# Kernel tuning notes

Hardware: AMD Instinct MI355X
Metric: run time of the kernel (lower is better)

## Reference

```python
import jax, jax.numpy as jnp
import numpy as np

B, H, S, D = 2, 16, 2048, 64

def setup_inputs() -> dict:
    key = jax.random.key(0)
    kq, kk, kv = jax.random.split(key, 3)
    q = jax.random.normal(kq, (B, H, S, D), dtype=jnp.float32)
    k = jax.random.normal(kk, (B, H, S, D), dtype=jnp.float32)
    v = jax.random.normal(kv, (B, H, S, D), dtype=jnp.float32)
    mask = jnp.tril(jnp.ones((S, S), dtype=bool))  # causal, broadcast over B,H
    return {"q": q, "k": k, "v": v, "mask": mask}

def reference(q, k, v, mask):
    d_k = q.shape[-1]
    # [..., num_q, num_kv]
    qk = jnp.einsum('bhqd,bhkd->bhqk', q, k) / jnp.sqrt(jnp.asarray(d_k, q.dtype))
    qk = jnp.where(mask, qk, -jnp.inf)
    attn = jax.nn.softmax(qk, axis=-1)
    return jnp.einsum('bhqk,bhkd->bhqd', attn, v)
```

## Files before the change

kernel.cpp:

```cpp
#include <hip/hip_runtime.h>

#define SS 2048
#define DD 64
#define BH 32
#define QSCALE 0.1803368801f
#define BUFS 8448

typedef __attribute__((ext_vector_type(8))) short short8;
typedef __attribute__((ext_vector_type(4))) float floatx4;

__device__ __forceinline__ short f2bf(float x) {
  union { float f; unsigned u; } un; un.f = x;
  unsigned r = (un.u + 0x7FFFu + ((un.u >> 16) & 1u)) >> 16;
  return (short)r;
}
__device__ __forceinline__ float fexp2(float x) {
  return __builtin_amdgcn_exp2f(x);
}
__device__ __forceinline__ void gload16(const short* g, short* l) {
  __builtin_amdgcn_global_load_lds(
      (const __attribute__((address_space(1))) void*)g,
      (__attribute__((address_space(3))) void*)l, 16, 0, 0);
}
#define MFMA __builtin_amdgcn_mfma_f32_16x16x32_bf16

__device__ __forceinline__ int kperm(int c) {
  return (((c >> 2) & 1) << 4) + ((c >> 3) << 2) + (c & 3);
}

__global__ __launch_bounds__(256) void prep_kv(const float* __restrict__ K,
                                               const float* __restrict__ V,
                                               short* __restrict__ Kbf,
                                               short* __restrict__ Vtp) {
  __shared__ short Ts[64][72];
  const int bh = blockIdx.x;
  const int r0 = blockIdx.y * 64;
  const int t  = threadIdx.x;
  {
    const int r = t >> 2, c = (t & 3) * 16;
    const float* g = V + ((size_t)bh * SS + r0 + r) * DD + c;
    floatx4 a = *(const floatx4*)g;
    floatx4 b = *(const floatx4*)(g + 4);
    floatx4 cc = *(const floatx4*)(g + 8);
    floatx4 dd = *(const floatx4*)(g + 12);
    short8 x0, x1;
    x0[0]=f2bf(a[0]); x0[1]=f2bf(a[1]); x0[2]=f2bf(a[2]); x0[3]=f2bf(a[3]);
    x0[4]=f2bf(b[0]); x0[5]=f2bf(b[1]); x0[6]=f2bf(b[2]); x0[7]=f2bf(b[3]);
    x1[0]=f2bf(cc[0]);x1[1]=f2bf(cc[1]);x1[2]=f2bf(cc[2]);x1[3]=f2bf(cc[3]);
    x1[4]=f2bf(dd[0]);x1[5]=f2bf(dd[1]);x1[6]=f2bf(dd[2]);x1[7]=f2bf(dd[3]);
    *(short8*)&Ts[r][c] = x0;
    *(short8*)&Ts[r][c + 8] = x1;
  }
  {
    const size_t i = ((size_t)bh * SS + r0) * DD + (size_t)t * 16;
    floatx4 a = *(const floatx4*)(K + i);
    floatx4 b = *(const floatx4*)(K + i + 4);
    floatx4 cc = *(const floatx4*)(K + i + 8);
    floatx4 dd = *(const floatx4*)(K + i + 12);
    short8 x0, x1;
    x0[0]=f2bf(a[0]); x0[1]=f2bf(a[1]); x0[2]=f2bf(a[2]); x0[3]=f2bf(a[3]);
    x0[4]=f2bf(b[0]); x0[5]=f2bf(b[1]); x0[6]=f2bf(b[2]); x0[7]=f2bf(b[3]);
    x1[0]=f2bf(cc[0]);x1[1]=f2bf(cc[1]);x1[2]=f2bf(cc[2]);x1[3]=f2bf(cc[3]);
    x1[4]=f2bf(dd[0]);x1[5]=f2bf(dd[1]);x1[6]=f2bf(dd[2]);x1[7]=f2bf(dd[3]);
    *(short8*)(Kbf + i) = x0;
    *(short8*)(Kbf + i + 8) = x1;
  }
  __syncthreads();
  {
    const int d = t >> 2, cblk = (t & 3) * 16;
    short8 y0, y1;
    #pragma unroll
    for (int jj = 0; jj < 8; ++jj) {
      const int c0 = cblk + jj, c1 = cblk + 8 + jj;
      y0[jj] = Ts[(c0 & 32) + kperm(c0 & 31)][d];
      y1[jj] = Ts[(c1 & 32) + kperm(c1 & 31)][d];
    }
    const int kt  = (r0 + cblk) >> 5;
    const int kin = cblk & 31;
    short* o = Vtp + (((size_t)bh * 64 + kt) * 64 + d) * 32 + kin;
    *(short8*)o = y0;
    *(short8*)(o + 8) = y1;
  }
}

#define CVTPK(DST_, A_, B_) \
  __asm__("v_cvt_pk_bf16_f32 %0, %1, %2" : "=v"(DST_) : "v"(A_), "v"(B_))

#define TILE32(JJ, DIAG_)                                                    \
  {                                                                          \
    const short* lb = bufp + (JJ) * 2176;                                    \
    const short* vb = bufp + 4352 + (JJ) * 2048;                             \
    short8 kb00 = *(const short8*)(lb + kroA);                               \
    short8 kb01 = *(const short8*)(lb + kroB);                               \
    short8 kb10 = *(const short8*)(lb + kroA + 1088);                        \
    short8 kb11 = *(const short8*)(lb + kroB + 1088);                        \
    short8 vt0 = *(const short8*)(vb + vro);                                 \
    short8 vt1 = *(const short8*)(vb + vro + 512);                           \
    short8 vt2 = *(const short8*)(vb + vro + 1024);                          \
    short8 vt3 = *(const short8*)(vb + vro + 1536);                          \
    __builtin_amdgcn_s_setprio(1);                                           \
    floatx4 tA0 = z, tA1 = z, tB0 = z, tB1 = z;                              \
    tA0 = MFMA(kb00, qaA0, tA0, 0, 0, 0); tA0 = MFMA(kb01, qaA1, tA0, 0, 0, 0);\
    tA1 = MFMA(kb10, qaA0, tA1, 0, 0, 0); tA1 = MFMA(kb11, qaA1, tA1, 0, 0, 0);\
    tB0 = MFMA(kb00, qaB0, tB0, 0, 0, 0); tB0 = MFMA(kb01, qaB1, tB0, 0, 0, 0);\
    tB1 = MFMA(kb10, qaB0, tB1, 0, 0, 0); tB1 = MFMA(kb11, qaB1, tB1, 0, 0, 0);\
    if (DIAG_) {                                                             \
      _Pragma("unroll")                                                      \
      for (int r = 0; r < 4; ++r) {                                          \
        tA0[r] = (quad * 4 + r      <= l16) ? tA0[r] : -1e30f;               \
        tA1[r] = (quad * 4 + r + 16 <= l16) ? tA1[r] : -1e30f;               \
        tB1[r] = (quad * 4 + r      <= l16) ? tB1[r] : -1e30f;               \
      }                                                                      \
    }                                                                        \
    _Pragma("unroll")                                                        \
    for (int r = 0; r < 4; ++r) {                                            \
      tA0[r] = fexp2(tA0[r]); tA1[r] = fexp2(tA1[r]);                        \
      tB0[r] = fexp2(tB0[r]); tB1[r] = fexp2(tB1[r]);                        \
    }                                                                        \
    union { unsigned u[4]; short8 s; } upA, upB;                             \
    CVTPK(upA.u[0], tA0[0], tA0[1]); CVTPK(upA.u[1], tA0[2], tA0[3]);        \
    CVTPK(upA.u[2], tA1[0], tA1[1]); CVTPK(upA.u[3], tA1[2], tA1[3]);        \
    CVTPK(upB.u[0], tB0[0], tB0[1]); CVTPK(upB.u[1], tB0[2], tB0[3]);        \
    CVTPK(upB.u[2], tB1[0], tB1[1]); CVTPK(upB.u[3], tB1[2], tB1[3]);        \
    short8 paA = upA.s, paB = upB.s;                                         \
    sA = MFMA(ones, paA, sA, 0, 0, 0);                                       \
    sB = MFMA(ones, paB, sB, 0, 0, 0);                                       \
    oA0 = MFMA(vt0, paA, oA0, 0, 0, 0); oA1 = MFMA(vt1, paA, oA1, 0, 0, 0);  \
    oA2 = MFMA(vt2, paA, oA2, 0, 0, 0); oA3 = MFMA(vt3, paA, oA3, 0, 0, 0);  \
    oB0 = MFMA(vt0, paB, oB0, 0, 0, 0); oB1 = MFMA(vt1, paB, oB1, 0, 0, 0);  \
    oB2 = MFMA(vt2, paB, oB2, 0, 0, 0); oB3 = MFMA(vt3, paB, oB3, 0, 0, 0);  \
    __builtin_amdgcn_s_setprio(0);                                           \
  }

__global__ __launch_bounds__(256, 4) void sdpa_fused(
    const float* __restrict__ Q, const short* __restrict__ Kbf,
    const short* __restrict__ Vtp, float* __restrict__ Og) {
  __shared__ __align__(16) short Sh[2][BUFS];

  const int tid  = threadIdx.x;
  const int w    = tid >> 6;
  const int lane = tid & 63;
  const int quad = lane >> 4;
  const int l16  = lane & 15;
  const int qp   = w >> 1;
  const int kp   = w & 1;

  const int bh = blockIdx.x;
  const int y  = blockIdx.y;
  const int qt = (y < 16) ? (31 - y) : (y - 16);

  const size_t base = (size_t)bh * SS * DD;
  const short* kbase = Kbf + base;
  const short* vtb   = Vtp + base;

  const int kso = (lane >> 3) * 64 + (((lane & 7) ^ (lane >> 3)) * 8);
  const int vso = (lane >> 2) * 32 + (((lane & 3) ^ ((lane >> 3) & 3)) * 8);
  const int kroA = (l16 >> 3) * 544 + (l16 & 7) * 64 + ((quad ^ (l16 & 7)) * 8);
  const int kroB = (l16 >> 3) * 544 + (l16 & 7) * 64 + (((quad + 4) ^ (l16 & 7)) * 8);
  const int vro  = l16 * 32 + ((quad ^ ((l16 >> 1) & 3)) * 8);

  short8 ones;
  #pragma unroll
  for (int r = 0; r < 8; ++r) ones[r] = (short)0x3F80;
  const floatx4 z = {0.f, 0.f, 0.f, 0.f};

  const int np = qt + 1;
  const int qA = qt * 64 + qp * 32;
  const int qB = qA + 16;

  {
    const short* gk = kbase + w * 512 + kso;
    gload16(gk,        &Sh[0][w * 544]);
    gload16(gk + 2048, &Sh[0][2176 + w * 544]);
    const short* gv = vtb + w * 512 + vso;
    gload16(gv,        &Sh[0][4352 + w * 512]);
    gload16(gv + 2048, &Sh[0][6400 + w * 512]);
  }

  short8 qaA0, qaA1, qaB0, qaB1;
  {
    const float* ga = Q + base + (size_t)(qA + l16) * DD + quad * 8;
    const float* gb = Q + base + (size_t)(qB + l16) * DD + quad * 8;
    floatx4 a0 = *(const floatx4*)ga,        a1 = *(const floatx4*)(ga + 4);
    floatx4 a2 = *(const floatx4*)(ga + 32), a3 = *(const floatx4*)(ga + 36);
    floatx4 b0 = *(const floatx4*)gb,        b1 = *(const floatx4*)(gb + 4);
    floatx4 b2 = *(const floatx4*)(gb + 32), b3 = *(const floatx4*)(gb + 36);
    #pragma unroll
    for (int r = 0; r < 4; ++r) {
      qaA0[r] = f2bf(a0[r] * QSCALE); qaA0[4 + r] = f2bf(a1[r] * QSCALE);
      qaA1[r] = f2bf(a2[r] * QSCALE); qaA1[4 + r] = f2bf(a3[r] * QSCALE);
      qaB0[r] = f2bf(b0[r] * QSCALE); qaB0[4 + r] = f2bf(b1[r] * QSCALE);
      qaB1[r] = f2bf(b2[r] * QSCALE); qaB1[4 + r] = f2bf(b3[r] * QSCALE);
    }
  }

  floatx4 oA0 = z, oA1 = z, oA2 = z, oA3 = z;
  floatx4 oB0 = z, oB1 = z, oB2 = z, oB3 = z;
  floatx4 sA = z, sB = z;

  int nb = 0;
  for (int p = 0; p < np; ++p) {
    __asm__ volatile("s_waitcnt vmcnt(0)" ::: "memory");
    __syncthreads();
    const short* bufp = Sh[nb];

    if (p + 1 < np) {
      {
        const size_t go = (size_t)(p + 1) * 4096;
        const short* gk = kbase + go + w * 512 + kso;
        gload16(gk,        &Sh[nb ^ 1][w * 544]);
        gload16(gk + 2048, &Sh[nb ^ 1][2176 + w * 544]);
        const short* gv = vtb + go + w * 512 + vso;
        gload16(gv,        &Sh[nb ^ 1][4352 + w * 512]);
        gload16(gv + 2048, &Sh[nb ^ 1][6400 + w * 512]);
      }
      TILE32(kp, 0)
    } else {
      if (kp == qp) { TILE32(kp, 1) }
      else if (kp < qp) { TILE32(kp, 0) }
    }
    nb ^= 1;
  }

  __syncthreads();
  float* lf = (float*)&Sh[0][0];
  if (kp) {
    floatx4* dst = (floatx4*)&lf[qp * 2048];
    dst[0 * 64 + lane] = oA0; dst[1 * 64 + lane] = oA1;
    dst[2 * 64 + lane] = oA2; dst[3 * 64 + lane] = oA3;
    dst[4 * 64 + lane] = oB0; dst[5 * 64 + lane] = oB1;
    dst[6 * 64 + lane] = oB2; dst[7 * 64 + lane] = oB3;
    lf[4096 + qp * 128 + lane]      = sA[0];
    lf[4096 + qp * 128 + 64 + lane] = sB[0];
  }
  __syncthreads();
  if (!kp) {
    const floatx4* src = (const floatx4*)&lf[qp * 2048];
    oA0 += src[0 * 64 + lane]; oA1 += src[1 * 64 + lane];
    oA2 += src[2 * 64 + lane]; oA3 += src[3 * 64 + lane];
    oB0 += src[4 * 64 + lane]; oB1 += src[5 * 64 + lane];
    oB2 += src[6 * 64 + lane]; oB3 += src[7 * 64 + lane];
    const float invA = 1.0f / (sA[0] + lf[4096 + qp * 128 + lane]);
    const float invB = 1.0f / (sB[0] + lf[4096 + qp * 128 + 64 + lane]);
    oA0 *= invA; oA1 *= invA; oA2 *= invA; oA3 *= invA;
    oB0 *= invB; oB1 *= invB; oB2 *= invB; oB3 *= invB;
    float* ra = Og + base + (size_t)(qA + l16) * DD + quad * 4;
    float* rb = Og + base + (size_t)(qB + l16) * DD + quad * 4;
    *(floatx4*)(ra)      = oA0;
    *(floatx4*)(ra + 16) = oA1;
    *(floatx4*)(ra + 32) = oA2;
    *(floatx4*)(ra + 48) = oA3;
    *(floatx4*)(rb)      = oB0;
    *(floatx4*)(rb + 16) = oB1;
    *(floatx4*)(rb + 32) = oB2;
    *(floatx4*)(rb + 48) = oB3;
  }
}

extern "C" void kernel_launch(void* const* d_in, const int* in_sizes, int n_in,
                              void* d_out, int out_size, void* d_ws, size_t ws_size,
                              hipStream_t stream) {
  (void)in_sizes; (void)n_in; (void)out_size; (void)ws_size;
  const float* q = (const float*)d_in[0];
  const float* k = (const float*)d_in[1];
  const float* v = (const float*)d_in[2];
  float* o = (float*)d_out;

  short* Kbf = (short*)d_ws;
  short* Vtp = Kbf + (size_t)BH * SS * DD;

  prep_kv<<<dim3(BH, SS / 64), 256, 0, stream>>>(k, v, Kbf, Vtp);
  sdpa_fused<<<dim3(BH, 32), 256, 0, stream>>>(q, Kbf, Vtp, o);
}
```

Before: 131.1 us.

## Load K/V fragments directly from global memory, dropping LDS double buffering

```diff
diff --git a/kernel.cpp b/kernel.cpp
--- a/kernel.cpp
+++ b/kernel.cpp
@@ -4,7 +4,6 @@
 #define DD 64
 #define BH 32
 #define QSCALE 0.1803368801f
-#define BUFS 8448
 
 typedef __attribute__((ext_vector_type(8))) short short8;
 typedef __attribute__((ext_vector_type(4))) float floatx4;
@@ -16,11 +15,6 @@
 }
 __device__ __forceinline__ float fexp2(float x) {
   return __builtin_amdgcn_exp2f(x);
-}
-__device__ __forceinline__ void gload16(const short* g, short* l) {
-  __builtin_amdgcn_global_load_lds(
-      (const __attribute__((address_space(1))) void*)g,
-      (__attribute__((address_space(3))) void*)l, 16, 0, 0);
 }
 #define MFMA __builtin_amdgcn_mfma_f32_16x16x32_bf16
 
@@ -86,18 +80,18 @@
 #define CVTPK(DST_, A_, B_) \
   __asm__("v_cvt_pk_bf16_f32 %0, %1, %2" : "=v"(DST_) : "v"(A_), "v"(B_))
 
-#define TILE32(JJ, DIAG_)                                                    \
+#define TILE32(KT_, DIAG_)                                                   \
   {                                                                          \
-    const short* lb = bufp + (JJ) * 2176;                                    \
-    const short* vb = bufp + 4352 + (JJ) * 2048;                             \
-    short8 kb00 = *(const short8*)(lb + kroA);                               \
-    short8 kb01 = *(const short8*)(lb + kroB);                               \
-    short8 kb10 = *(const short8*)(lb + kroA + 1088);                        \
-    short8 kb11 = *(const short8*)(lb + kroB + 1088);                        \
-    short8 vt0 = *(const short8*)(vb + vro);                                 \
-    short8 vt1 = *(const short8*)(vb + vro + 512);                           \
-    short8 vt2 = *(const short8*)(vb + vro + 1024);                          \
-    short8 vt3 = *(const short8*)(vb + vro + 1536);                          \
+    const short* kg = kbase + (size_t)(KT_) * 2048;                          \
+    const short* vg = vtb   + (size_t)(KT_) * 2048;                          \
+    short8 kb00 = *(const short8*)(kg + kofs);                               \
+    short8 kb01 = *(const short8*)(kg + kofs + 32);                          \
+    short8 kb10 = *(const short8*)(kg + kofs + 1024);                        \
+    short8 kb11 = *(const short8*)(kg + kofs + 1056);                        \
+    short8 vt0 = *(const short8*)(vg + vofs);                                \
+    short8 vt1 = *(const short8*)(vg + vofs + 512);                          \
+    short8 vt2 = *(const short8*)(vg + vofs + 1024);                         \
+    short8 vt3 = *(const short8*)(vg + vofs + 1536);                         \
     __builtin_amdgcn_s_setprio(1);                                           \
     floatx4 tA0 = z, tA1 = z, tB0 = z, tB1 = z;                              \
     tA0 = MFMA(kb00, qaA0, tA0, 0, 0, 0); tA0 = MFMA(kb01, qaA1, tA0, 0, 0, 0);\
@@ -135,7 +129,7 @@
 __global__ __launch_bounds__(256, 4) void sdpa_fused(
     const float* __restrict__ Q, const short* __restrict__ Kbf,
     const short* __restrict__ Vtp, float* __restrict__ Og) {
-  __shared__ __align__(16) short Sh[2][BUFS];
+  __shared__ __align__(16) float lf[4352];
 
   const int tid  = threadIdx.x;
   const int w    = tid >> 6;
@@ -153,29 +147,16 @@
   const short* kbase = Kbf + base;
   const short* vtb   = Vtp + base;
 
-  const int kso = (lane >> 3) * 64 + (((lane & 7) ^ (lane >> 3)) * 8);
-  const int vso = (lane >> 2) * 32 + (((lane & 3) ^ ((lane >> 3) & 3)) * 8);
-  const int kroA = (l16 >> 3) * 544 + (l16 & 7) * 64 + ((quad ^ (l16 & 7)) * 8);
-  const int kroB = (l16 >> 3) * 544 + (l16 & 7) * 64 + (((quad + 4) ^ (l16 & 7)) * 8);
-  const int vro  = l16 * 32 + ((quad ^ ((l16 >> 1) & 3)) * 8);
+  const int kofs = l16 * 64 + quad * 8;
+  const int vofs = l16 * 32 + quad * 8;
 
   short8 ones;
   #pragma unroll
   for (int r = 0; r < 8; ++r) ones[r] = (short)0x3F80;
   const floatx4 z = {0.f, 0.f, 0.f, 0.f};
 
-  const int np = qt + 1;
   const int qA = qt * 64 + qp * 32;
   const int qB = qA + 16;
-
-  {
-    const short* gk = kbase + w * 512 + kso;
-    gload16(gk,        &Sh[0][w * 544]);
-    gload16(gk + 2048, &Sh[0][2176 + w * 544]);
-    const short* gv = vtb + w * 512 + vso;
-    gload16(gv,        &Sh[0][4352 + w * 512]);
-    gload16(gv + 2048, &Sh[0][6400 + w * 512]);
-  }
 
   short8 qaA0, qaA1, qaB0, qaB1;
   {
@@ -198,32 +179,18 @@
   floatx4 oB0 = z, oB1 = z, oB2 = z, oB3 = z;
   floatx4 sA = z, sB = z;
 
-  int nb = 0;
-  for (int p = 0; p < np; ++p) {
-    __asm__ volatile("s_waitcnt vmcnt(0)" ::: "memory");
-    __syncthreads();
-    const short* bufp = Sh[nb];
-
-    if (p + 1 < np) {
-      {
-        const size_t go = (size_t)(p + 1) * 4096;
-        const short* gk = kbase + go + w * 512 + kso;
-        gload16(gk,        &Sh[nb ^ 1][w * 544]);
-        gload16(gk + 2048, &Sh[nb ^ 1][2176 + w * 544]);
-        const short* gv = vtb + go + w * 512 + vso;
-        gload16(gv,        &Sh[nb ^ 1][4352 + w * 512]);
-        gload16(gv + 2048, &Sh[nb ^ 1][6400 + w * 512]);
-      }
-      TILE32(kp, 0)
-    } else {
-      if (kp == qp) { TILE32(kp, 1) }
-      else if (kp < qp) { TILE32(kp, 0) }
-    }
-    nb ^= 1;
+  const int nt = (kp == 1 && qp == 0) ? qt : (qt + 1);
+  const int ndiag = (kp == qp) ? (nt - 1) : nt;
+
+  #pragma unroll 2
+  for (int i = 0; i < ndiag; ++i) {
+    TILE32(2 * i + kp, 0)
+  }
+  if (kp == qp) {
+    TILE32(2 * (nt - 1) + kp, 1)
   }
 
   __syncthreads();
-  float* lf = (float*)&Sh[0][0];
   if (kp) {
     floatx4* dst = (floatx4*)&lf[qp * 2048];
     dst[0 * 64 + lane] = oA0; dst[1 * 64 + lane] = oA1;
```

New measurement: 155.9 us. 18.9% more time.
